# Kernel tuning notes

Measured on AMD Instinct MI355X. Metric: run time of the kernel, lower is better.

Reference implementation:

```python
import jax, jax.numpy as jnp
import numpy as np
import math

DIM = 1024
N_HEADS = 16
HEAD_DIM = DIM // N_HEADS
MAX_SEQ_LEN = 2048


def rope_tables(seq_len, head_dim):
    inv_freq = 1.0 / (10000.0 ** (jnp.arange(0, head_dim, 2, dtype=jnp.float32) / head_dim))
    t = jnp.arange(seq_len, dtype=jnp.float32)
    freqs = jnp.einsum('i,j->ij', t, inv_freq)          # [T, D/2]
    emb = jnp.concatenate([freqs, freqs], axis=-1)      # [T, D]
    return jnp.cos(emb), jnp.sin(emb)


def rotate_half(x):
    x1, x2 = jnp.split(x, 2, axis=-1)
    return jnp.concatenate([-x2, x1], axis=-1)


def setup_inputs() -> dict:
    key = jax.random.key(0)
    k1, k2, k3 = jax.random.split(key, 3)
    B, T = 4, 2048
    x = jax.random.normal(k1, (B, T, DIM), dtype=jnp.float32)
    # Linear(dim, 3*dim, bias=False) and Linear(dim, dim, bias=False); stored as [in, out]
    Wqkv = jax.random.normal(k2, (DIM, 3 * DIM), dtype=jnp.float32) * (1.0 / math.sqrt(DIM))
    Wproj = jax.random.normal(k3, (DIM, DIM), dtype=jnp.float32) * (1.0 / math.sqrt(DIM))
    return {"x": x, "Wqkv": Wqkv, "Wproj": Wproj}


def reference(x, Wqkv, Wproj):
    B, T, C = x.shape
    qkv = x @ Wqkv                                       # [B,T,3C]
    q, k, v = jnp.split(qkv, 3, axis=-1)
    # [B,T,C] -> [B,H,T,D]
    def to_heads(t_):
        return t_.reshape(B, T, N_HEADS, HEAD_DIM).transpose(0, 2, 1, 3)
    q, k, v = to_heads(q), to_heads(k), to_heads(v)
    cos, sin = rope_tables(T, HEAD_DIM)                  # [T,D]
    cos = cos[None, None, :, :]
    sin = sin[None, None, :, :]
    q = q * cos + rotate_half(q) * sin
    k = k * cos + rotate_half(k) * sin
    scale = 1.0 / math.sqrt(HEAD_DIM)
    att = jnp.einsum('bhqd,bhkd->bhqk', q, k) * scale    # [B,H,T,T]
    causal = jnp.triu(jnp.ones((T, T), dtype=bool), k=1)
    att = jnp.where(causal[None, None], -jnp.inf, att)
    att = jax.nn.softmax(att, axis=-1)
    y = jnp.einsum('bhqk,bhkd->bhqd', att, v)            # [B,H,T,D]
    y = y.transpose(0, 2, 1, 3).reshape(B, T, C)
    return y @ Wproj
```

## Files before the change

kernel.cpp:

```cpp
#include <hip/hip_runtime.h>
#include <hip/hip_bf16.h>

typedef unsigned short u16;
typedef __attribute__((ext_vector_type(8))) short short8;
typedef __attribute__((ext_vector_type(4))) float floatx4;

__device__ __forceinline__ u16 f2bf(float f) {
    union { float f; unsigned u; } v; v.f = f;
    unsigned r = v.u + 0x7fffu + ((v.u >> 16) & 1u);
    return (u16)(r >> 16);
}
__device__ __forceinline__ float fexp2(float x) {
#if __has_builtin(__builtin_amdgcn_exp2f)
    return __builtin_amdgcn_exp2f(x);
#else
    return exp2f(x);
#endif
}

__device__ __forceinline__ void async_load16(const void* g, void* l) {
    __builtin_amdgcn_global_load_lds(
        (const __attribute__((address_space(1))) unsigned int*)g,
        (__attribute__((address_space(3))) unsigned int*)l, 16, 0, 0);
}

#define B_   4
#define T_   2048
#define NH_  16
#define HD_  64
#define DIM_ 1024
#define M_   (B_ * T_)
#define NQKV (3 * DIM_)
#define NT_  16
#define LOG2E 1.4426950408889634f

__global__ void cvt_x(const float* __restrict__ in, u16* __restrict__ out) {
    int idx = blockIdx.x * 256 + threadIdx.x;
    float4 v = ((const float4*)in)[idx];
    ushort4 o;
    o.x = f2bf(v.x); o.y = f2bf(v.y); o.z = f2bf(v.z); o.w = f2bf(v.w);
    ((ushort4*)out)[idx] = o;
}

__global__ void transpose_cvt(const float* __restrict__ in, u16* __restrict__ out,
                              int R, int Cn) {
    __shared__ float tile[32][33];
    int c0 = blockIdx.x * 32, r0 = blockIdx.y * 32;
    int tx = threadIdx.x, ty = threadIdx.y;
#pragma unroll
    for (int i = 0; i < 4; ++i)
        tile[ty + i * 8][tx] = in[(size_t)(r0 + ty + i * 8) * Cn + c0 + tx];
    __syncthreads();
#pragma unroll
    for (int i = 0; i < 4; ++i)
        out[(size_t)(c0 + ty + i * 8) * R + r0 + tx] = f2bf(tile[tx][ty + i * 8]);
}

__global__ void rope_table(float* __restrict__ tabc, float* __restrict__ tabs) {
    int idx = blockIdx.x * 256 + threadIdx.x;
    if (idx >= T_ * 32) return;
    int t = idx >> 5, j = idx & 31;
    double invf = pow(10000.0, -(double)j / 32.0);
    double th = (double)t * invf;
    tabc[idx] = (float)cos(th);
    tabs[idx] = (float)sin(th);
}

__global__ void v_transpose(const u16* __restrict__ Vh, u16* __restrict__ Vt) {
    __shared__ u16 tile[64 * 68];
    const int tid = threadIdx.x;
    const int bh = blockIdx.y, b = bh >> 4, h = bh & 15;
    const int t0 = blockIdx.x * 64;
    {
        int lr = tid >> 2;
        int lc = tid & 3;
        const u16* src = Vh + ((size_t)(b * T_ + t0 + lr)) * DIM_ + h * HD_;
#pragma unroll
        for (int j = 0; j < 4; ++j) {
            int c = (lc + j * 4) * 4;
            *(uint2*)&tile[lr * 68 + c] = *(const uint2*)(src + c);
        }
    }
    __syncthreads();
    {
        int d2 = tid >> 3, tseg = tid & 7;
        u16 lo8[8], hi8[8];
#pragma unroll
        for (int j = 0; j < 8; ++j) {
            unsigned w = *(const unsigned*)&tile[(tseg * 8 + j) * 68 + d2 * 2];
            lo8[j] = (u16)(w & 0xffffu);
            hi8[j] = (u16)(w >> 16);
        }
        size_t ob = ((size_t)bh * HD_ + 2 * d2) * T_ + t0 + tseg * 8;
        *(uint4*)(Vt + ob) = *(const uint4*)lo8;
        *(uint4*)(Vt + ob + T_) = *(const uint4*)hi8;
    }
}

__device__ __forceinline__ void gemm_core(const u16* __restrict__ A,
                                          const u16* __restrict__ Bt,
                                          u16* smem, int m0, int n0, int tid,
                                          floatx4 (&acc)[4][4]) {
    const int wave = tid >> 6, lane = tid & 63;
    const int ln15 = lane & 15, quad = lane >> 4;
    const int wm = (wave & 1) * 64, wn = (wave >> 1) * 64;
    const int l8 = lane & 7, ld8 = lane >> 3;
    const int sgc = (l8 ^ ld8) * 8;
    const int K = DIM_;

    const u16* aS = A + (size_t)(m0 + wave * 16 + ld8) * K + sgc;
    const u16* bS = Bt + (size_t)(n0 + wave * 32 + ld8) * K + sgc;

    auto issueA_B0 = [&](int k2, u16* As2, u16* Bs2) {
        async_load16(aS + k2,          As2 + (wave * 16) * 64);
        async_load16(aS + 8 * K + k2,  As2 + (wave * 16 + 8) * 64);
        async_load16(bS + k2,          Bs2 + (wave * 32) * 64);
    };
    auto issueB123 = [&](int k2, u16* Bs2) {
        async_load16(bS + 8 * K + k2,  Bs2 + (wave * 32 + 8) * 64);
        async_load16(bS + 16 * K + k2, Bs2 + (wave * 32 + 16) * 64);
        async_load16(bS + 24 * K + k2, Bs2 + (wave * 32 + 24) * 64);
    };
    auto compute = [&](const u16* As_c, const u16* Bs_c, int c4) {
        short8 af[4], bfv[4];
#pragma unroll
        for (int i = 0; i < 4; ++i) {
            int row = wm + i * 16 + ln15;
            af[i] = *(const short8*)&As_c[row * 64 + (((c4 + quad) ^ (row & 7)) << 3)];
        }
#pragma unroll
        for (int j = 0; j < 4; ++j) {
            int row = wn + j * 16 + ln15;
            bfv[j] = *(const short8*)&Bs_c[row * 64 + (((c4 + quad) ^ (row & 7)) << 3)];
        }
        __builtin_amdgcn_s_setprio(1);
#pragma unroll
        for (int i = 0; i < 4; ++i)
#pragma unroll
            for (int j = 0; j < 4; ++j)
                acc[i][j] = __builtin_amdgcn_mfma_f32_16x16x32_bf16(
                    af[i], bfv[j], acc[i][j], 0, 0, 0);
        __builtin_amdgcn_s_setprio(0);
    };

    issueA_B0(0, smem, smem + 24576);
    issueB123(0, smem + 24576);
    issueA_B0(64, smem + 8192, smem + 24576 + 16384);
    issueB123(64, smem + 24576 + 16384);

#pragma unroll 1
    for (int t = 0; t < NT_; ++t) {
        if (t < NT_ - 1) asm volatile("s_waitcnt vmcnt(6)" ::: "memory");
        else             asm volatile("s_waitcnt vmcnt(0)" ::: "memory");
        __builtin_amdgcn_s_barrier();
        asm volatile("" ::: "memory");

        const int cb = t % 3, cb2 = (t + 2) % 3;
        const u16* As_c = smem + cb * 8192;
        const u16* Bs_c = smem + 24576 + cb * 16384;
        u16* As2 = smem + cb2 * 8192;
        u16* Bs2 = smem + 24576 + cb2 * 16384;
        const bool iss = t < NT_ - 2;
        const int k2 = (t + 2) * 64;

        if (iss) issueA_B0(k2, As2, Bs2);
        compute(As_c, Bs_c, 0);
        asm volatile("" ::: "memory");
        __builtin_amdgcn_s_barrier();
        asm volatile("" ::: "memory");

        if (iss) issueB123(k2, Bs2);
        compute(As_c, Bs_c, 4);
        asm volatile("" ::: "memory");
    }
}

__global__ __launch_bounds__(512, 2) void gemm_qkv(const u16* __restrict__ A,
                                                   const u16* __restrict__ Bt,
                                                   const float* __restrict__ tabc,
                                                   const float* __restrict__ tabs,
                                                   u16* __restrict__ Qo,
                                                   u16* __restrict__ Ko,
                                                   u16* __restrict__ Vh) {
    __shared__ __align__(16) u16 smem[73728];
    const int tid = threadIdx.x;
    const int bid = blockIdx.x;
    const int wg = (bid & 7) * 96 + (bid >> 3);
    const int bx = wg / 64, by = wg - bx * 64;
    const int m0 = by * 128, n0 = bx * 256;

    floatx4 acc[4][4] = {};
    gemm_core(A, Bt, smem, m0, n0, tid, acc);

    const int wave = tid >> 6, lane = tid & 63;
    const int ln15 = lane & 15, quad = lane >> 4;
    const int wm = (wave & 1) * 64, wn = (wave >> 1) * 64;

    __syncthreads();
    u16* Es = smem;
    const int sel = n0 >> 10;
    auto es_put = [&](int row, int col, u16 v) {
        int c = col >> 3;
        int pc = (c & 24) | ((c & 7) ^ (row & 7));
        Es[row * 256 + pc * 8 + (col & 7)] = v;
    };
    if (sel == 2) {
#pragma unroll
        for (int i = 0; i < 4; ++i)
#pragma unroll
            for (int j = 0; j < 4; ++j)
#pragma unroll
                for (int r = 0; r < 4; ++r)
                    es_put(wm + i * 16 + quad * 4 + r, wn + j * 16 + ln15,
                           f2bf(acc[i][j][r]));
    } else {
        const float scale = sel ? 1.0f : 0.125f * LOG2E;
#pragma unroll
        for (int i = 0; i < 4; ++i)
#pragma unroll
            for (int jjl = 0; jjl < 2; ++jjl) {
                int j = jjl * 16 + ln15;
#pragma unroll
                for (int r = 0; r < 4; ++r) {
                    int row = wm + i * 16 + quad * 4 + r;
                    int t = (m0 + row) & (T_ - 1);
                    float cs = tabc[t * 32 + j], sn = tabs[t * 32 + j];
                    float xl = acc[i][jjl][r], xh = acc[i][jjl + 2][r];
                    es_put(row, wn + j,      f2bf((xl * cs - xh * sn) * scale));
                    es_put(row, wn + j + 32, f2bf((xh * cs + xl * sn) * scale));
                }
            }
    }
    __syncthreads();
    const int bb = m0 >> 11;
    u16* outqk = (sel == 1) ? Ko : Qo;
#pragma unroll
    for (int k = 0; k < 8; ++k) {
        int cid = tid + k * 512;
        int row = cid >> 5, c = cid & 31;
        int pc = (c & 24) | ((c & 7) ^ (row & 7));
        uint4 v = *(const uint4*)&Es[row * 256 + pc * 8];
        if (sel == 2) {
            *(uint4*)&Vh[(size_t)(m0 + row) * DIM_ + (n0 & 1023) + c * 8] = v;
        } else {
            int h = ((n0 & 1023) >> 6) + (c >> 3);
            int d = (c & 7) * 8;
            int t = (m0 + row) & (T_ - 1);
            *(uint4*)&outqk[((size_t)(bb * NH_ + h) * T_ + t) * HD_ + d] = v;
        }
    }
}

__global__ __launch_bounds__(512, 2) void gemm_proj(const u16* __restrict__ A,
                                                    const u16* __restrict__ Bt,
                                                    float* __restrict__ C) {
    __shared__ __align__(16) u16 smem[73728];
    const int tid = threadIdx.x;
    const int bid = blockIdx.x;
    const int wg = (bid & 7) * 32 + (bid >> 3);
    const int bx = wg / 64, by = wg - bx * 64;
    const int m0 = by * 128, n0 = bx * 256;

    floatx4 acc[4][4] = {};
    gemm_core(A, Bt, smem, m0, n0, tid, acc);

    const int wave = tid >> 6, lane = tid & 63;
    const int ln15 = lane & 15, quad = lane >> 4;
    const int wm = (wave & 1) * 64, wn = (wave >> 1) * 64;
#pragma unroll
    for (int i = 0; i < 4; ++i)
#pragma unroll
        for (int j = 0; j < 4; ++j)
#pragma unroll
            for (int r = 0; r < 4; ++r) {
                int m = m0 + wm + i * 16 + quad * 4 + r;
                int n = n0 + wn + j * 16 + ln15;
                C[(size_t)m * DIM_ + n] = acc[i][j][r];
            }
}

__global__ __launch_bounds__(256, 4) void attn_kernel(const u16* __restrict__ Q,
                                                      const u16* __restrict__ Kh,
                                                      const u16* __restrict__ Vt,
                                                      u16* __restrict__ Y) {
    __shared__ __align__(16) u16 Kl[2][64 * 64];
    __shared__ __align__(16) u16 Vl[2][64 * 64];
    __shared__ __align__(16) u16 Pl[4][16 * 64];
    const int tid = threadIdx.x, wave = tid >> 6, lane = tid & 63;
    const int ln15 = lane & 15, quad = lane >> 4;
    const int p = blockIdx.x;
    const int bh = blockIdx.y;
    const int b = bh >> 4, h = bh & 15;
    const int l8 = lane & 7, ld8 = lane >> 3;
    const int sgc = l8 ^ ld8;

    const u16* kbase = Kh + (size_t)bh * T_ * HD_;
    const u16* vbase = Vt + (size_t)bh * HD_ * T_;
    const short8 ones = {0x3F80, 0x3F80, 0x3F80, 0x3F80,
                         0x3F80, 0x3F80, 0x3F80, 0x3F80};
    const int srow = wave * 16;

#pragma unroll
    for (int half = 0; half < 2; ++half) {
        const int tidx = half ? p : (31 - p);
        const int q0 = tidx * 64;
        const int bm = q0 + srow;

        const u16* qp = Q + ((size_t)bh * T_ + bm + ln15) * HD_;
        short8 qf0 = *(const short8*)(qp + quad * 8);
        short8 qf1 = *(const short8*)(qp + 32 + quad * 8);

        floatx4 o[5] = {};

        __syncthreads();
#pragma unroll
        for (int it = 0; it < 2; ++it) {
            int r = srow + it * 8;
            async_load16(kbase + (size_t)(r + ld8) * HD_ + sgc * 8, &Kl[0][r * 64]);
            async_load16(vbase + (size_t)(r + ld8) * T_ + sgc * 8, &Vl[0][r * 64]);
        }

        for (int kt = 0; kt <= tidx; ++kt) {
            const int cur = kt & 1;
            __syncthreads();
            if (kt < tidx) {
                const int kn = (kt + 1) * 64;
#pragma unroll
                for (int it = 0; it < 2; ++it) {
                    int r = srow + it * 8;
                    async_load16(kbase + (size_t)(kn + r + ld8) * HD_ + sgc * 8,
                                 &Kl[cur ^ 1][r * 64]);
                    async_load16(vbase + (size_t)(r + ld8) * T_ + kn + sgc * 8,
                                 &Vl[cur ^ 1][r * 64]);
                }
            }
            floatx4 s[4] = {};
#pragma unroll
            for (int nt = 0; nt < 4; ++nt) {
                int row = nt * 16 + ln15;
                short8 kf0 = *(const short8*)&Kl[cur][row * 64 + ((quad ^ (row & 7)) << 3)];
                short8 kf1 = *(const short8*)&Kl[cur][row * 64 + (((4 + quad) ^ (row & 7)) << 3)];
                s[nt] = __builtin_amdgcn_mfma_f32_16x16x32_bf16(qf0, kf0, s[nt], 0, 0, 0);
                s[nt] = __builtin_amdgcn_mfma_f32_16x16x32_bf16(qf1, kf1, s[nt], 0, 0, 0);
            }
            if (kt == tidx) {
#pragma unroll
                for (int nt = 0; nt < 4; ++nt) {
                    int key = nt * 16 + ln15, lim = srow + quad * 4;
#pragma unroll
                    for (int r = 0; r < 4; ++r)
                        s[nt][r] = (key > lim + r) ? 0.f : fexp2(s[nt][r]);
                }
            } else {
#pragma unroll
                for (int nt = 0; nt < 4; ++nt)
#pragma unroll
                    for (int r = 0; r < 4; ++r) s[nt][r] = fexp2(s[nt][r]);
            }
            u16* pw = Pl[wave];
#pragma unroll
            for (int nt = 0; nt < 4; ++nt) {
                int kc = nt * 2 + (ln15 >> 3), k7 = ln15 & 7;
#pragma unroll
                for (int r = 0; r < 4; ++r) {
                    int row = quad * 4 + r;
                    pw[row * 64 + ((kc ^ (row & 7)) << 3) + k7] = f2bf(s[nt][r]);
                }
            }
            short8 pf0 = *(const short8*)&pw[ln15 * 64 + ((quad ^ (ln15 & 7)) << 3)];
            short8 pf1 = *(const short8*)&pw[ln15 * 64 + (((4 + quad) ^ (ln15 & 7)) << 3)];
#pragma unroll
            for (int nt = 0; nt < 4; ++nt) {
                int row = nt * 16 + ln15;
                short8 vf0 = *(const short8*)&Vl[cur][row * 64 + ((quad ^ (row & 7)) << 3)];
                short8 vf1 = *(const short8*)&Vl[cur][row * 64 + (((4 + quad) ^ (row & 7)) << 3)];
                o[nt] = __builtin_amdgcn_mfma_f32_16x16x32_bf16(pf0, vf0, o[nt], 0, 0, 0);
                o[nt] = __builtin_amdgcn_mfma_f32_16x16x32_bf16(pf1, vf1, o[nt], 0, 0, 0);
            }
            o[4] = __builtin_amdgcn_mfma_f32_16x16x32_bf16(pf0, ones, o[4], 0, 0, 0);
            o[4] = __builtin_amdgcn_mfma_f32_16x16x32_bf16(pf1, ones, o[4], 0, 0, 0);
        }
#pragma unroll
        for (int r = 0; r < 4; ++r) {
            float inv = 1.f / o[4][r];
            int row = bm + quad * 4 + r;
            u16* yp = Y + ((size_t)(b * T_ + row)) * DIM_ + h * HD_;
#pragma unroll
            for (int nt = 0; nt < 4; ++nt)
                yp[nt * 16 + ln15] = f2bf(o[nt][r] * inv);
        }
    }
}

extern "C" void kernel_launch(void* const* d_in, const int* in_sizes, int n_in,
                              void* d_out, int out_size, void* d_ws, size_t ws_size,
                              hipStream_t stream) {
    const float* x     = (const float*)d_in[0];
    const float* Wqkv  = (const float*)d_in[1];
    const float* Wproj = (const float*)d_in[2];
    float* out = (float*)d_out;
    char* ws = (char*)d_ws;

    const size_t SZ_XB  = (size_t)M_ * DIM_ * 2;
    const size_t SZ_WQT = (size_t)NQKV * DIM_ * 2;
    const size_t SZ_WPT = (size_t)DIM_ * DIM_ * 2;
    const size_t SZ_Q   = SZ_XB;
    const size_t SZ_TAB = (size_t)T_ * 32 * 4;

    u16*   xb   = (u16*)(ws);
    u16*   wqt  = (u16*)(ws + SZ_XB);
    u16*   wpt  = (u16*)(ws + SZ_XB + SZ_WQT);
    u16*   qb   = (u16*)(ws + SZ_XB + SZ_WQT + SZ_WPT);
    u16*   kb   = (u16*)(ws + SZ_XB + SZ_WQT + SZ_WPT + SZ_Q);
    u16*   vhb  = (u16*)(ws + SZ_XB + SZ_WQT + SZ_WPT + 2 * SZ_Q);
    u16*   vtb  = (u16*)(ws + SZ_XB + SZ_WQT + SZ_WPT + 3 * SZ_Q);
    float* tabc = (float*)(ws + SZ_XB + SZ_WQT + SZ_WPT + 4 * SZ_Q);
    float* tabs = (float*)(ws + SZ_XB + SZ_WQT + SZ_WPT + 4 * SZ_Q + SZ_TAB);
    u16*   yb   = xb;

    rope_table<<<(T_ * 32 + 255) / 256, 256, 0, stream>>>(tabc, tabs);
    cvt_x<<<(M_ * DIM_ / 4) / 256, 256, 0, stream>>>(x, xb);
    transpose_cvt<<<dim3(NQKV / 32, DIM_ / 32), dim3(32, 8), 0, stream>>>(Wqkv, wqt, DIM_, NQKV);
    transpose_cvt<<<dim3(DIM_ / 32, DIM_ / 32), dim3(32, 8), 0, stream>>>(Wproj, wpt, DIM_, DIM_);
    gemm_qkv<<<768, 512, 0, stream>>>(xb, wqt, tabc, tabs, qb, kb, vhb);
    v_transpose<<<dim3(T_ / 64, B_ * NH_), 256, 0, stream>>>(vhb, vtb);
    attn_kernel<<<dim3(16, B_ * NH_), 256, 0, stream>>>(qb, kb, vtb, yb);
    gemm_proj<<<256, 512, 0, stream>>>(yb, wpt, out);
}
```

Before: 262.8 us.

## Keep attention P in registers via transposed S and permlane swaps

Computes the score tile transposed (K as the A operand) so each lane's exp values can be packed to bf16 with v_cvt_pk and rearranged with permlane32/16 swaps into the A-operand layout for the PV MFMA. This removes the per-tile LDS write and read of P and frees that shared memory. The change also raises MFMA issue priority with s_setprio, raises launch_bounds occupancy to 5, and flattens the grid with an XCD-aware block remap. Correctness depends on the register permutation matching the MFMA fragment layout exactly.

After: 239.9 us. -8.7%, faster.

```diff
diff --git a/kernel.cpp b/kernel.cpp
--- a/kernel.cpp
+++ b/kernel.cpp
@@ -16,6 +16,17 @@
 #else
     return exp2f(x);
 #endif
+}
+__device__ __forceinline__ unsigned cvtpk_bf16(float lo, float hi) {
+    unsigned r;
+    asm("v_cvt_pk_bf16_f32 %0, %1, %2" : "=v"(r) : "v"(lo), "v"(hi));
+    return r;
+}
+__device__ __forceinline__ void permlane32_swap(unsigned &a, unsigned &b) {
+    asm("v_permlane32_swap_b32 %0, %1" : "+v"(a), "+v"(b));
+}
+__device__ __forceinline__ void permlane16_swap(unsigned &a, unsigned &b) {
+    asm("v_permlane16_swap_b32 %0, %1" : "+v"(a), "+v"(b));
 }
 
 __device__ __forceinline__ void async_load16(const void* g, void* l) {
@@ -279,17 +290,18 @@
             }
 }
 
-__global__ __launch_bounds__(256, 4) void attn_kernel(const u16* __restrict__ Q,
+__global__ __launch_bounds__(256, 5) void attn_kernel(const u16* __restrict__ Q,
                                                       const u16* __restrict__ Kh,
                                                       const u16* __restrict__ Vt,
                                                       u16* __restrict__ Y) {
     __shared__ __align__(16) u16 Kl[2][64 * 64];
     __shared__ __align__(16) u16 Vl[2][64 * 64];
-    __shared__ __align__(16) u16 Pl[4][16 * 64];
     const int tid = threadIdx.x, wave = tid >> 6, lane = tid & 63;
     const int ln15 = lane & 15, quad = lane >> 4;
-    const int p = blockIdx.x;
-    const int bh = blockIdx.y;
+    const int bid = blockIdx.x;
+    const int wg = (bid & 7) * 128 + (bid >> 3);
+    const int p = wg & 15;
+    const int bh = wg >> 4;
     const int b = bh >> 4, h = bh & 15;
     const int l8 = lane & 7, ld8 = lane >> 3;
     const int sgc = l8 ^ ld8;
@@ -335,21 +347,24 @@
                 }
             }
             floatx4 s[4] = {};
+            __builtin_amdgcn_s_setprio(1);
 #pragma unroll
             for (int nt = 0; nt < 4; ++nt) {
                 int row = nt * 16 + ln15;
                 short8 kf0 = *(const short8*)&Kl[cur][row * 64 + ((quad ^ (row & 7)) << 3)];
                 short8 kf1 = *(const short8*)&Kl[cur][row * 64 + (((4 + quad) ^ (row & 7)) << 3)];
-                s[nt] = __builtin_amdgcn_mfma_f32_16x16x32_bf16(qf0, kf0, s[nt], 0, 0, 0);
-                s[nt] = __builtin_amdgcn_mfma_f32_16x16x32_bf16(qf1, kf1, s[nt], 0, 0, 0);
-            }
+                s[nt] = __builtin_amdgcn_mfma_f32_16x16x32_bf16(kf0, qf0, s[nt], 0, 0, 0);
+                s[nt] = __builtin_amdgcn_mfma_f32_16x16x32_bf16(kf1, qf1, s[nt], 0, 0, 0);
+            }
+            __builtin_amdgcn_s_setprio(0);
             if (kt == tidx) {
+                const int lim = srow + ln15;
 #pragma unroll
                 for (int nt = 0; nt < 4; ++nt) {
-                    int key = nt * 16 + ln15, lim = srow + quad * 4;
+                    int key = nt * 16 + quad * 4;
 #pragma unroll
                     for (int r = 0; r < 4; ++r)
-                        s[nt][r] = (key > lim + r) ? 0.f : fexp2(s[nt][r]);
+                        s[nt][r] = (key + r > lim) ? 0.f : fexp2(s[nt][r]);
                 }
             } else {
 #pragma unroll
@@ -357,28 +372,33 @@
 #pragma unroll
                     for (int r = 0; r < 4; ++r) s[nt][r] = fexp2(s[nt][r]);
             }
-            u16* pw = Pl[wave];
-#pragma unroll
-            for (int nt = 0; nt < 4; ++nt) {
-                int kc = nt * 2 + (ln15 >> 3), k7 = ln15 & 7;
-#pragma unroll
-                for (int r = 0; r < 4; ++r) {
-                    int row = quad * 4 + r;
-                    pw[row * 64 + ((kc ^ (row & 7)) << 3) + k7] = f2bf(s[nt][r]);
-                }
-            }
-            short8 pf0 = *(const short8*)&pw[ln15 * 64 + ((quad ^ (ln15 & 7)) << 3)];
-            short8 pf1 = *(const short8*)&pw[ln15 * 64 + (((4 + quad) ^ (ln15 & 7)) << 3)];
+            unsigned x0 = cvtpk_bf16(s[0][0], s[0][1]);
+            unsigned x1 = cvtpk_bf16(s[1][0], s[1][1]);
+            unsigned y0 = cvtpk_bf16(s[0][2], s[0][3]);
+            unsigned y1 = cvtpk_bf16(s[1][2], s[1][3]);
+            unsigned x2 = cvtpk_bf16(s[2][0], s[2][1]);
+            unsigned x3 = cvtpk_bf16(s[3][0], s[3][1]);
+            unsigned y2 = cvtpk_bf16(s[2][2], s[2][3]);
+            unsigned y3 = cvtpk_bf16(s[3][2], s[3][3]);
+            permlane32_swap(x0, x1); permlane16_swap(x0, x1);
+            permlane32_swap(y0, y1); permlane16_swap(y0, y1);
+            permlane32_swap(x2, x3); permlane16_swap(x2, x3);
+            permlane32_swap(y2, y3); permlane16_swap(y2, y3);
+            union { unsigned u[4]; short8 s8; } pk0, pk1;
+            pk0.u[0] = x0; pk0.u[1] = y0; pk0.u[2] = x1; pk0.u[3] = y1;
+            pk1.u[0] = x2; pk1.u[1] = y2; pk1.u[2] = x3; pk1.u[3] = y3;
+            __builtin_amdgcn_s_setprio(1);
 #pragma unroll
             for (int nt = 0; nt < 4; ++nt) {
                 int row = nt * 16 + ln15;
                 short8 vf0 = *(const short8*)&Vl[cur][row * 64 + ((quad ^ (row & 7)) << 3)];
                 short8 vf1 = *(const short8*)&Vl[cur][row * 64 + (((4 + quad) ^ (row & 7)) << 3)];
-                o[nt] = __builtin_amdgcn_mfma_f32_16x16x32_bf16(pf0, vf0, o[nt], 0, 0, 0);
-                o[nt] = __builtin_amdgcn_mfma_f32_16x16x32_bf16(pf1, vf1, o[nt], 0, 0, 0);
-            }
-            o[4] = __builtin_amdgcn_mfma_f32_16x16x32_bf16(pf0, ones, o[4], 0, 0, 0);
-            o[4] = __builtin_amdgcn_mfma_f32_16x16x32_bf16(pf1, ones, o[4], 0, 0, 0);
+                o[nt] = __builtin_amdgcn_mfma_f32_16x16x32_bf16(pk0.s8, vf0, o[nt], 0, 0, 0);
+                o[nt] = __builtin_amdgcn_mfma_f32_16x16x32_bf16(pk1.s8, vf1, o[nt], 0, 0, 0);
+            }
+            o[4] = __builtin_amdgcn_mfma_f32_16x16x32_bf16(pk0.s8, ones, o[4], 0, 0, 0);
+            o[4] = __builtin_amdgcn_mfma_f32_16x16x32_bf16(pk1.s8, ones, o[4], 0, 0, 0);
+            __builtin_amdgcn_s_setprio(0);
         }
 #pragma unroll
         for (int r = 0; r < 4; ++r) {
@@ -424,6 +444,6 @@
     transpose_cvt<<<dim3(DIM_ / 32, DIM_ / 32), dim3(32, 8), 0, stream>>>(Wproj, wpt, DIM_, DIM_);
     gemm_qkv<<<768, 512, 0, stream>>>(xb, wqt, tabc, tabs, qb, kb, vhb);
     v_transpose<<<dim3(T_ / 64, B_ * NH_), 256, 0, stream>>>(vhb, vtb);
-    attn_kernel<<<dim3(16, B_ * NH_), 256, 0, stream>>>(qb, kb, vtb, yb);
+    attn_kernel<<<1024, 256, 0, stream>>>(qb, kb, vtb, yb);
     gemm_proj<<<256, 512, 0, stream>>>(yb, wpt, out);
 }
```
